# Kernel tuning notes

Measured on AMD Instinct MI355X. Metric: run time of the kernel, lower is better.

Reference implementation:

```python
import jax, jax.numpy as jnp
import numpy as np
from jax import lax

K = 3
STRIDE = 1
PAD = 1
DIL = 1
C_IN = 64
C_OUT = 128


def setup_inputs() -> dict:
    key = jax.random.key(0)
    k1, k2, k3, k4 = jax.random.split(key, 4)
    x = jax.random.normal(k1, (4, C_IN, 64, 256), dtype=jnp.float32)
    # offset/mask conv params (zero-init in the module; small random so sampling is exercised)
    offset_weight = jax.random.normal(k2, (3 * K * K, C_IN, K, K), dtype=jnp.float32) * 0.02
    offset_bias = jax.random.normal(k3, (3 * K * K,), dtype=jnp.float32) * 0.02
    # main deformable conv weight (kaiming_uniform a=1 -> uniform(+-sqrt(3/fan_in)/..); scale approx)
    fan_in = C_IN * K * K
    weight = jax.random.normal(k4, (C_OUT, C_IN, K, K), dtype=jnp.float32) * (1.0 / np.sqrt(fan_in))
    return {"x": x, "offset_weight": offset_weight, "offset_bias": offset_bias, "weight": weight}


def _deform_conv2d(x, offset, mask, weight):
    """torchvision.ops.deform_conv2d (v2, with mask) semantics.
    x: [B,C,H,W], offset: [B,2*K*K,Ho,Wo] interleaved (dy,dx) per tap,
    mask: [B,K*K,Ho,Wo], weight: [O,C,K,K]."""
    B, C, H, W = x.shape
    O = weight.shape[0]
    KK = K * K
    Ho, Wo = mask.shape[2], mask.shape[3]

    off = offset.reshape(B, KK, 2, Ho, Wo)
    dy, dx = off[:, :, 0], off[:, :, 1]  # [B,KK,Ho,Wo]

    ki = jnp.repeat(jnp.arange(K), K)   # kernel row per tap, [KK]
    kj = jnp.tile(jnp.arange(K), K)     # kernel col per tap, [KK]

    # sampling positions
    py = dy + (jnp.arange(Ho) * STRIDE - PAD)[None, None, :, None] + (ki * DIL)[None, :, None, None]
    px = dx + (jnp.arange(Wo) * STRIDE - PAD)[None, None, None, :] + (kj * DIL)[None, :, None, None]

    y0f = jnp.floor(py)
    x0f = jnp.floor(px)
    ly = py - y0f
    lx = px - x0f
    y0 = y0f.astype(jnp.int32)
    x0 = x0f.astype(jnp.int32)

    x_flat = x.reshape(B, C, H * W)

    def gather(yy, xx, w):
        valid = (yy >= 0) & (yy < H) & (xx >= 0) & (xx < W)
        idx = jnp.clip(yy, 0, H - 1) * W + jnp.clip(xx, 0, W - 1)
        v = jax.vmap(lambda xf, ix: jnp.take(xf, ix, axis=1))(x_flat, idx.reshape(B, -1))
        v = v.reshape(B, C, KK, Ho, Wo)
        return v * (w * valid)[:, None]  # zero outside image (zero padding)

    samp = gather(y0, x0, (1.0 - ly) * (1.0 - lx))
    samp = samp + gather(y0, x0 + 1, (1.0 - ly) * lx)
    samp = samp + gather(y0 + 1, x0, ly * (1.0 - lx))
    samp = samp + gather(y0 + 1, x0 + 1, ly * lx)

    samp = samp * mask[:, None]  # modulation
    # contract over input channels and kernel taps
    return jnp.einsum('bckhw,ock->bohw', samp, weight.reshape(O, C, KK))


def reference(x, offset_weight, offset_bias, weight):
    om = lax.conv_general_dilated(
        x, offset_weight,
        window_strides=(STRIDE, STRIDE),
        padding=[(PAD, PAD), (PAD, PAD)],
        rhs_dilation=(DIL, DIL),
        dimension_numbers=('NCHW', 'OIHW', 'NCHW'),
    ) + offset_bias[None, :, None, None]
    KK = K * K
    o1, o2, m = om[:, :KK], om[:, KK:2 * KK], om[:, 2 * KK:]
    offset = jnp.concatenate([o1, o2], axis=1)
    mask = jax.nn.sigmoid(m)
    return _deform_conv2d(x, offset, mask, weight)
```

## Files before the change

kernel.cpp:

```cpp
#include <hip/hip_runtime.h>
#include <math.h>

#define BB   4
#define CIN  64
#define HH   64
#define WW   256
#define CO   128
#define NPIX (BB*HH*WW)

typedef float  f32x4 __attribute__((ext_vector_type(4)));
typedef unsigned int u32x4 __attribute__((ext_vector_type(4)));
typedef _Float16 f16x8 __attribute__((ext_vector_type(8)));
typedef _Float16 f16x2 __attribute__((ext_vector_type(2)));

#define XTB_OFF  0
#define XTB_SZ   (NPIX*32)
#define OWB_OFF  (XTB_OFF + XTB_SZ)
#define OWB_SZ   9216
#define WTF_OFF  (OWB_OFF + OWB_SZ)


__device__ inline int xcd_swz(int bid)    { return (bid & 7) * 128 + (bid >> 3); }
__device__ inline int xcd_swz256(int bid) { return (bid & 7) * 32  + (bid >> 3); }

__global__ __launch_bounds__(256) void k_prep(const float* __restrict__ x,
                                              const float* __restrict__ ow,
                                              const float* __restrict__ wm,
                                              unsigned int* __restrict__ xtb,
                                              unsigned short* __restrict__ owb,
                                              unsigned short* __restrict__ wtF) {
    __shared__ float t[64][65];
    int tid = threadIdx.x;
    if (blockIdx.x < 1024) {
        int bx = xcd_swz(blockIdx.x);
        int x0 = (bx & 3) * 64;
        int y  = (bx >> 2) & 63;
        int b  = bx >> 8;
        int lx = tid & 63, gy = tid >> 6;
#pragma unroll
        for (int i = 0; i < 16; ++i) {
            int c = i * 4 + gy;
            t[c][lx] = x[((b*CIN + c)*HH + y)*WW + x0 + lx];
        }
        __syncthreads();
        int px = tid & 63, cg = tid >> 6;
        u32x4 r0, r1;
#pragma unroll
        for (int j = 0; j < 4; ++j) {
            f16x2 p, q;
            p[0] = (_Float16)t[cg*16 + 2*j][px];
            p[1] = (_Float16)t[cg*16 + 2*j + 1][px];
            q[0] = (_Float16)t[cg*16 + 8 + 2*j][px];
            q[1] = (_Float16)t[cg*16 + 8 + 2*j + 1][px];
            r0[j] = __builtin_bit_cast(unsigned int, p);
            r1[j] = __builtin_bit_cast(unsigned int, q);
        }
        int xx = x0 + px;
        int u = ((b*HH + y)*16 + (xx >> 4))*128 + (xx & 15);
        u32x4* dst = (u32x4*)xtb;
        dst[u + (2*cg)*16]     = r0;
        dst[u + (2*cg + 1)*16] = r1;
    } else {
        const int n1 = 18432;
        const int n2 = 9*CO*CIN;
        for (int i = (blockIdx.x - 1024)*256 + tid; i < n1 + n2; i += 16*256) {
            if (i < n1) {
                int j = i & 7, l = (i >> 3) & 63, mi = (i >> 9) & 1, kk = i >> 10;
                int oc = mi*16 + (l & 15);
                int k  = kk*32 + (l >> 4)*8 + j;
                int tt = k >> 6, c = k & 63;
                float v = (oc < 27) ? ow[(oc*CIN + c)*9 + tt] : 0.f;
                owb[i] = __builtin_bit_cast(unsigned short, (_Float16)v);
            } else {
                int j = i - n1;
                int k = j / (CO*CIN);
                int r = j % (CO*CIN);
                int o = r / CIN, c = r % CIN;
                float v = wm[(o*CIN + c)*9 + k];
                wtF[k*8192 + (r ^ ((o & 7) << 3))] =
                    __builtin_bit_cast(unsigned short, (_Float16)v);
            }
        }
    }
}

__device__ inline f16x8 lerp8h(u32x4 a, u32x4 b, u32x4 c, u32x4 d,
                               f16x8 w0, f16x8 w1, f16x8 w2, f16x8 w3) {
    f16x8 av = __builtin_bit_cast(f16x8, a);
    f16x8 bv = __builtin_bit_cast(f16x8, b);
    f16x8 cv = __builtin_bit_cast(f16x8, c);
    f16x8 dv = __builtin_bit_cast(f16x8, d);
    return av*w0 + bv*w1 + cv*w2 + dv*w3;
}

__device__ inline f16x8 splat8(float s) {
    _Float16 h = (_Float16)s;
    return (f16x8){h, h, h, h, h, h, h, h};
}

__global__ __launch_bounds__(1024, 4) void k_fused(const unsigned int* __restrict__ xtb,
                                                   const unsigned short* __restrict__ owb,
                                                   const float* __restrict__ ob,
                                                   const unsigned short* __restrict__ wtF,
                                                   float* __restrict__ out) {
    __shared__ u32x4 wlds[9216];
    __shared__ _Float16 pscr[7168];
    int bx = xcd_swz256(blockIdx.x);
    int ho = bx & 63, b = bx >> 6;
    int tid = threadIdx.x;
    int w = tid >> 6;
    int l = tid & 63;
    int pxl = l & 15, hi = l >> 4;
    int wo = w*16 + pxl;

    const u32x4* xtb4 = (const u32x4*)xtb;
    int pbase = (w*16 + pxl) * 28;

    {
        const u32x4* asrc = (const u32x4*)owb;
        f32x4 acc0 = (f32x4){0.f,0.f,0.f,0.f}, acc1 = (f32x4){0.f,0.f,0.f,0.f};
#pragma unroll
        for (int kk = 0; kk < 18; ++kk) {
            const int t = kk >> 1;
            const int ki = t / 3, kj = t % 3;
            int y  = ho + ki - 1;
            int xx = wo + kj - 1;
            bool v = (y >= 0) && (y < HH) && (xx >= 0) && (xx < WW);
            int yc = min(max(y, 0), HH-1), xc = min(max(xx, 0), WW-1);
            u32x4 bv = xtb4[((b*HH + yc)*16 + (xc >> 4))*128
                            + ((kk & 1)*4 + hi)*16 + (xc & 15)];
            if (!v) bv = (u32x4){0u,0u,0u,0u};
            u32x4 a0 = asrc[(kk*2+0)*64 + l];
            u32x4 a1 = asrc[(kk*2+1)*64 + l];
            __builtin_amdgcn_s_setprio(1);
            acc0 = __builtin_amdgcn_mfma_f32_16x16x32_f16(
                       __builtin_bit_cast(f16x8, a0), __builtin_bit_cast(f16x8, bv), acc0, 0, 0, 0);
            acc1 = __builtin_amdgcn_mfma_f32_16x16x32_f16(
                       __builtin_bit_cast(f16x8, a1), __builtin_bit_cast(f16x8, bv), acc1, 0, 0, 0);
            __builtin_amdgcn_s_setprio(0);
        }
#pragma unroll
        for (int r = 0; r < 4; ++r) {
            int oc0 = hi*4 + r;
            float v0 = acc0[r] + ob[oc0];
            pscr[pbase + (oc0 & 1)*9 + (oc0 >> 1)] = (_Float16)v0;
            int oc1 = 16 + hi*4 + r;
            if (oc1 < 27) {
                float v1 = acc1[r] + ob[oc1];
                if (oc1 < 18) pscr[pbase + (oc1 & 1)*9 + (oc1 >> 1)] = (_Float16)v1;
                else          pscr[pbase + oc1] = (_Float16)(1.f / (1.f + __expf(-v1)));
            }
        }
    }

    const u32x4* wsrc = (const u32x4*)wtF;
#pragma unroll
    for (int i = 0; i < 9; ++i) wlds[tid + i*1024] = wsrc[tid + i*1024];

    int lo0 = (hi*16)      ^ ((l & 7) << 4);
    int lo1 = (64 + hi*16) ^ ((l & 7) << 4);
    int abase = pxl * 128;

    int   idx[2][4];
    float wts[2][4];
    u32x4 G[2][4];
    float pdy0, pdx0, pm0, pdy1, pdx1, pm1;

    auto load_par0 = [&](int k) { pdy0 = (float)pscr[pbase+k]; pdx0 = (float)pscr[pbase+9+k]; pm0 = (float)pscr[pbase+18+k]; };
    auto load_par1 = [&](int k) { pdy1 = (float)pscr[pbase+k]; pdx1 = (float)pscr[pbase+9+k]; pm1 = (float)pscr[pbase+18+k]; };

    auto tap_addr = [&](int k, float dy, float dx, float m) {
        int ki = k / 3, kj = k - ki*3;
        float py  = dy + (float)(ho - 1 + ki);
        float pxf = dx + (float)(wo - 1 + kj);
        float y0f = floorf(py), x0f = floorf(pxf);
        float ly = py - y0f, lxf = pxf - x0f;
        int y0 = (int)y0f, x0 = (int)x0f;
        int y1 = y0 + 1,  x1 = x0 + 1;
        bool vy0 = (y0 >= 0) && (y0 < HH), vy1 = (y1 >= 0) && (y1 < HH);
        bool vx0 = (x0 >= 0) && (x0 < WW), vx1 = (x1 >= 0) && (x1 < WW);
        float hy = 1.f - ly, hx = 1.f - lxf;
        int s = k & 1;
        wts[s][0] = (vy0 && vx0) ? hy*hx*m : 0.f;
        wts[s][1] = (vy0 && vx1) ? hy*lxf*m : 0.f;
        wts[s][2] = (vy1 && vx0) ? ly*hx*m : 0.f;
        wts[s][3] = (vy1 && vx1) ? ly*lxf*m : 0.f;
        int yc0 = min(max(y0, 0), HH-1), yc1 = min(max(y1, 0), HH-1);
        int xc0 = min(max(x0, 0), WW-1), xc1 = min(max(x1, 0), WW-1);
        int rb0 = (b*HH + yc0)*16, rb1 = (b*HH + yc1)*16;
        idx[s][0] = (rb0 + (xc0 >> 4))*128 + (xc0 & 15);
        idx[s][1] = (rb0 + (xc1 >> 4))*128 + (xc1 & 15);
        idx[s][2] = (rb1 + (xc0 >> 4))*128 + (xc0 & 15);
        idx[s][3] = (rb1 + (xc1 >> 4))*128 + (xc1 & 15);
    };

    auto issue_half = [&](int h) {
        int k = h >> 1, p = h & 1;
        const int* id = idx[k & 1];
        u32x4* g = G[h & 1];
        int ch = (p*4 + hi) * 16;
        g[0] = xtb4[id[0] + ch];
        g[1] = xtb4[id[1] + ch];
        g[2] = xtb4[id[2] + ch];
        g[3] = xtb4[id[3] + ch];
    };

    load_par0(0);
    tap_addr(0, pdy0, pdx0, pm0);
    load_par1(1);
    issue_half(0);

    asm volatile("s_waitcnt lgkmcnt(0)\n\ts_barrier" ::: "memory");

    f32x4 acc[8];
#pragma unroll
    for (int i = 0; i < 8; ++i) acc[i] = (f32x4){0.f, 0.f, 0.f, 0.f};

#pragma unroll
    for (int h = 0; h < 18; ++h) {
        const int t = h >> 1, p = h & 1;
        if ((h & 1) && (t + 1 < 9)) {
            if ((t + 1) & 1) tap_addr(t + 1, pdy1, pdx1, pm1);
            else             tap_addr(t + 1, pdy0, pdx0, pm0);
            if (t + 2 < 9) {
                if ((t + 2) & 1) load_par1(t + 2);
                else             load_par0(t + 2);
            }
        }
        if (h + 1 < 18) issue_half(h + 1);

        const float* W = wts[t & 1];
        f16x8 bf = lerp8h(G[h & 1][0], G[h & 1][1], G[h & 1][2], G[h & 1][3],
                          splat8(W[0]), splat8(W[1]), splat8(W[2]), splat8(W[3]));
        const char* wb = (const char*)wlds + t*16384;
        const int lo = p ? lo1 : lo0;
        __builtin_amdgcn_s_setprio(1);
#pragma unroll
        for (int mi = 0; mi < 8; ++mi) {
            u32x4 a = *(const u32x4*)(wb + (abase + lo + mi*2048));
            acc[mi] = __builtin_amdgcn_mfma_f32_16x16x32_f16(
                          __builtin_bit_cast(f16x8, a), bf, acc[mi], 0, 0, 0);
        }
        __builtin_amdgcn_s_setprio(0);
    }

#pragma unroll
    for (int mi = 0; mi < 8; ++mi) {
#pragma unroll
        for (int r = 0; r < 4; ++r) {
            int o = mi*16 + hi*4 + r;
            out[((b*CO + o)*HH + ho)*WW + wo] = acc[mi][r];
        }
    }
}

extern "C" void kernel_launch(void* const* d_in, const int* in_sizes, int n_in,
                              void* d_out, int out_size, void* d_ws, size_t ws_size,
                              hipStream_t stream) {
    const float* x  = (const float*)d_in[0];
    const float* ow = (const float*)d_in[1];
    const float* ob = (const float*)d_in[2];
    const float* wm = (const float*)d_in[3];
    float* outp = (float*)d_out;

    float* ws   = (float*)d_ws;
    unsigned int* xtb = (unsigned int*)(ws + XTB_OFF);
    unsigned short* owb = (unsigned short*)(ws + OWB_OFF);
    unsigned short* wtF = (unsigned short*)(ws + WTF_OFF);

    k_prep<<<1040, 256, 0, stream>>>(x, ow, wm, xtb, owb, wtF);
    k_fused<<<256, 1024, 0, stream>>>(xtb, owb, ob, wtF, outp);
}
```

Measured before the change: 41.58 us.

## Switch fused deformable conv to 32x32x16 MFMA with 512-thread blocks

Replaces the 16x16x32 MFMA tiling in both the offset conv and the main deformable conv with 32x32x16 MFMA. Each wave now covers 32 output pixels, and blocks shrink to 512 threads (8 waves) per row. The prep kernel rewrites the weight layouts to match the new A-fragment order and drops the XOR swizzle. The larger tiles reuse each bilinear-sampled B fragment across more output channels and cut the number of MFMA issues. In exchange, each thread handles more K-steps with more gathers and lerps, occupancy per block is lower, and LDS fragment reads are no longer swizzled.

```diff
diff --git a/kernel.cpp b/kernel.cpp
--- a/kernel.cpp
+++ b/kernel.cpp
@@ -9,6 +9,7 @@
 #define NPIX (BB*HH*WW)
 
 typedef float  f32x4 __attribute__((ext_vector_type(4)));
+typedef float  f32x16 __attribute__((ext_vector_type(16)));
 typedef unsigned int u32x4 __attribute__((ext_vector_type(4)));
 typedef _Float16 f16x8 __attribute__((ext_vector_type(8)));
 typedef _Float16 f16x2 __attribute__((ext_vector_type(2)));
@@ -65,20 +66,19 @@
         const int n2 = 9*CO*CIN;
         for (int i = (blockIdx.x - 1024)*256 + tid; i < n1 + n2; i += 16*256) {
             if (i < n1) {
-                int j = i & 7, l = (i >> 3) & 63, mi = (i >> 9) & 1, kk = i >> 10;
-                int oc = mi*16 + (l & 15);
-                int k  = kk*32 + (l >> 4)*8 + j;
-                int tt = k >> 6, c = k & 63;
+                int j = i & 7, l = (i >> 3) & 63, s = (i >> 9) & 3, tt = i >> 11;
+                int oc = l & 31;
+                int c  = s*16 + (l >> 5)*8 + j;
                 float v = (oc < 27) ? ow[(oc*CIN + c)*9 + tt] : 0.f;
                 owb[i] = __builtin_bit_cast(unsigned short, (_Float16)v);
             } else {
-                int j = i - n1;
-                int k = j / (CO*CIN);
-                int r = j % (CO*CIN);
-                int o = r / CIN, c = r % CIN;
-                float v = wm[(o*CIN + c)*9 + k];
-                wtF[k*8192 + (r ^ ((o & 7) << 3))] =
-                    __builtin_bit_cast(unsigned short, (_Float16)v);
+                int jj = i - n1;
+                int j = jj & 7, l = (jj >> 3) & 63, f = (jj >> 9) & 3;
+                int s = (jj >> 11) & 3, tt = jj >> 13;
+                int oc = f*32 + (l & 31);
+                int c  = s*16 + (l >> 5)*8 + j;
+                float v = wm[(oc*CIN + c)*9 + tt];
+                wtF[jj] = __builtin_bit_cast(unsigned short, (_Float16)v);
             }
         }
     }
@@ -98,11 +98,11 @@
     return (f16x8){h, h, h, h, h, h, h, h};
 }
 
-__global__ __launch_bounds__(1024, 4) void k_fused(const unsigned int* __restrict__ xtb,
-                                                   const unsigned short* __restrict__ owb,
-                                                   const float* __restrict__ ob,
-                                                   const unsigned short* __restrict__ wtF,
-                                                   float* __restrict__ out) {
+__global__ __launch_bounds__(512, 2) void k_fused(const unsigned int* __restrict__ xtb,
+                                                  const unsigned short* __restrict__ owb,
+                                                  const float* __restrict__ ob,
+                                                  const unsigned short* __restrict__ wtF,
+                                                  float* __restrict__ out) {
     __shared__ u32x4 wlds[9216];
     __shared__ _Float16 pscr[7168];
     int bx = xcd_swz256(blockIdx.x);
@@ -110,56 +110,51 @@
     int tid = threadIdx.x;
     int w = tid >> 6;
     int l = tid & 63;
-    int pxl = l & 15, hi = l >> 4;
-    int wo = w*16 + pxl;
+    int pxw = l & 31, khalf = l >> 5;
+    int wo = w*32 + pxw;
 
     const u32x4* xtb4 = (const u32x4*)xtb;
-    int pbase = (w*16 + pxl) * 28;
+    int pbase = wo * 28;
 
     {
         const u32x4* asrc = (const u32x4*)owb;
-        f32x4 acc0 = (f32x4){0.f,0.f,0.f,0.f}, acc1 = (f32x4){0.f,0.f,0.f,0.f};
-#pragma unroll
-        for (int kk = 0; kk < 18; ++kk) {
-            const int t = kk >> 1;
-            const int ki = t / 3, kj = t % 3;
+        f32x16 accA;
+#pragma unroll
+        for (int i = 0; i < 16; ++i) accA[i] = 0.f;
+#pragma unroll
+        for (int t = 0; t < 9; ++t) {
+            int ki = t / 3, kj = t % 3;
             int y  = ho + ki - 1;
             int xx = wo + kj - 1;
             bool v = (y >= 0) && (y < HH) && (xx >= 0) && (xx < WW);
             int yc = min(max(y, 0), HH-1), xc = min(max(xx, 0), WW-1);
-            u32x4 bv = xtb4[((b*HH + yc)*16 + (xc >> 4))*128
-                            + ((kk & 1)*4 + hi)*16 + (xc & 15)];
-            if (!v) bv = (u32x4){0u,0u,0u,0u};
-            u32x4 a0 = asrc[(kk*2+0)*64 + l];
-            u32x4 a1 = asrc[(kk*2+1)*64 + l];
-            __builtin_amdgcn_s_setprio(1);
-            acc0 = __builtin_amdgcn_mfma_f32_16x16x32_f16(
-                       __builtin_bit_cast(f16x8, a0), __builtin_bit_cast(f16x8, bv), acc0, 0, 0, 0);
-            acc1 = __builtin_amdgcn_mfma_f32_16x16x32_f16(
-                       __builtin_bit_cast(f16x8, a1), __builtin_bit_cast(f16x8, bv), acc1, 0, 0, 0);
-            __builtin_amdgcn_s_setprio(0);
-        }
-#pragma unroll
-        for (int r = 0; r < 4; ++r) {
-            int oc0 = hi*4 + r;
-            float v0 = acc0[r] + ob[oc0];
-            pscr[pbase + (oc0 & 1)*9 + (oc0 >> 1)] = (_Float16)v0;
-            int oc1 = 16 + hi*4 + r;
-            if (oc1 < 27) {
-                float v1 = acc1[r] + ob[oc1];
-                if (oc1 < 18) pscr[pbase + (oc1 & 1)*9 + (oc1 >> 1)] = (_Float16)v1;
-                else          pscr[pbase + oc1] = (_Float16)(1.f / (1.f + __expf(-v1)));
+            int cb = ((b*HH + yc)*16 + (xc >> 4))*128 + (xc & 15);
+#pragma unroll
+            for (int s = 0; s < 4; ++s) {
+                u32x4 bv = xtb4[cb + (s*2 + khalf)*16];
+                if (!v) bv = (u32x4){0u,0u,0u,0u};
+                u32x4 a = asrc[(t*4 + s)*64 + l];
+                __builtin_amdgcn_s_setprio(1);
+                accA = __builtin_amdgcn_mfma_f32_32x32x16_f16(
+                           __builtin_bit_cast(f16x8, a), __builtin_bit_cast(f16x8, bv),
+                           accA, 0, 0, 0);
+                __builtin_amdgcn_s_setprio(0);
+            }
+        }
+#pragma unroll
+        for (int r = 0; r < 16; ++r) {
+            int row = (r & 3) + 8*(r >> 2) + 4*khalf;
+            if (row < 27) {
+                float v = accA[r] + ob[row];
+                if (row < 18) pscr[pbase + (row & 1)*9 + (row >> 1)] = (_Float16)v;
+                else          pscr[pbase + row] = (_Float16)(1.f / (1.f + __expf(-v)));
             }
         }
     }
 
     const u32x4* wsrc = (const u32x4*)wtF;
 #pragma unroll
-    for (int i = 0; i < 9; ++i) wlds[tid + i*1024] = wsrc[tid + i*1024];
-
-    int lo0 = (hi*16)      ^ ((l & 7) << 4);
-    int lo1 = (64 + hi*16) ^ ((l & 7) << 4);
-    int abase = pxl * 128;
+    for (int i = 0; i < 18; ++i) wlds[tid + i*512] = wsrc[tid + i*512];
 
     int   idx[2][4];
     float wts[2][4];
@@ -194,32 +189,34 @@
         idx[s][3] = (rb1 + (xc1 >> 4))*128 + (xc1 & 15);
     };
 
-    auto issue_half = [&](int h) {
-        int k = h >> 1, p = h & 1;
-        const int* id = idx[k & 1];
-        u32x4* g = G[h & 1];
-        int ch = (p*4 + hi) * 16;
-        g[0] = xtb4[id[0] + ch];
-        g[1] = xtb4[id[1] + ch];
-        g[2] = xtb4[id[2] + ch];
-        g[3] = xtb4[id[3] + ch];
+    auto issue_ks = [&](int ss) {
+        int t = ss >> 2, s = ss & 3;
+        const int* id = idx[t & 1];
+        u32x4* g = G[ss & 1];
+        int oct = (s*2 + khalf) * 16;
+        g[0] = xtb4[id[0] + oct];
+        g[1] = xtb4[id[1] + oct];
+        g[2] = xtb4[id[2] + oct];
+        g[3] = xtb4[id[3] + oct];
     };
 
     load_par0(0);
     tap_addr(0, pdy0, pdx0, pm0);
     load_par1(1);
-    issue_half(0);
+    issue_ks(0);
 
     asm volatile("s_waitcnt lgkmcnt(0)\n\ts_barrier" ::: "memory");
 
-    f32x4 acc[8];
-#pragma unroll
-    for (int i = 0; i < 8; ++i) acc[i] = (f32x4){0.f, 0.f, 0.f, 0.f};
-
-#pragma unroll
-    for (int h = 0; h < 18; ++h) {
-        const int t = h >> 1, p = h & 1;
-        if ((h & 1) && (t + 1 < 9)) {
+    f32x16 acc[4];
+#pragma unroll
+    for (int f = 0; f < 4; ++f)
+#pragma unroll
+        for (int i = 0; i < 16; ++i) acc[f][i] = 0.f;
+
+#pragma unroll
+    for (int ss = 0; ss < 36; ++ss) {
+        const int t = ss >> 2, s = ss & 3;
+        if (s == 3 && t + 1 < 9) {
             if ((t + 1) & 1) tap_addr(t + 1, pdy1, pdx1, pm1);
             else             tap_addr(t + 1, pdy0, pdx0, pm0);
             if (t + 2 < 9) {
@@ -227,31 +224,28 @@
                 else             load_par0(t + 2);
             }
         }
-        if (h + 1 < 18) issue_half(h + 1);
+        if (ss + 1 < 36) issue_ks(ss + 1);
 
         const float* W = wts[t & 1];
-        f16x8 bf = lerp8h(G[h & 1][0], G[h & 1][1], G[h & 1][2], G[h & 1][3],
+        f16x8 bf = lerp8h(G[ss & 1][0], G[ss & 1][1], G[ss & 1][2], G[ss & 1][3],
                           splat8(W[0]), splat8(W[1]), splat8(W[2]), splat8(W[3]));
-        const char* wb = (const char*)wlds + t*16384;
-        const int lo = p ? lo1 : lo0;
         __builtin_amdgcn_s_setprio(1);
 #pragma unroll
-        for (int mi = 0; mi < 8; ++mi) {
-            u32x4 a = *(const u32x4*)(wb + (abase + lo + mi*2048));
-            acc[mi] = __builtin_amdgcn_mfma_f32_16x16x32_f16(
-                          __builtin_bit_cast(f16x8, a), bf, acc[mi], 0, 0, 0);
+        for (int f = 0; f < 4; ++f) {
+            u32x4 a = wlds[((t*4 + s)*4 + f)*64 + l];
+            acc[f] = __builtin_amdgcn_mfma_f32_32x32x16_f16(
+                         __builtin_bit_cast(f16x8, a), bf, acc[f], 0, 0, 0);
         }
         __builtin_amdgcn_s_setprio(0);
     }
 
 #pragma unroll
-    for (int mi = 0; mi < 8; ++mi) {
-#pragma unroll
-        for (int r = 0; r < 4; ++r) {
-            int o = mi*16 + hi*4 + r;
-            out[((b*CO + o)*HH + ho)*WW + wo] = acc[mi][r];
-        }
-    }
+    for (int f = 0; f < 4; ++f)
+#pragma unroll
+        for (int r = 0; r < 16; ++r) {
+            int o = f*32 + (r & 3) + 8*(r >> 2) + 4*khalf;
+            out[((b*CO + o)*HH + ho)*WW + wo] = acc[f][r];
+        }
 }
 
 extern "C" void kernel_launch(void* const* d_in, const int* in_sizes, int n_in,
@@ -269,5 +263,5 @@
     unsigned short* wtF = (unsigned short*)(ws + WTF_OFF);
 
     k_prep<<<1040, 256, 0, stream>>>(x, ow, wm, xtb, owb, wtF);
-    k_fused<<<256, 1024, 0, stream>>>(xtb, owb, ob, wtF, outp);
-}
+    k_fused<<<256, 512, 0, stream>>>(xtb, owb, ob, wtF, outp);
+}
```

Result: slower. 44.55 us (+7.1%).
